# Kernel tuning notes

Hardware: AMD Instinct MI355X
Metric: run time of the kernel (lower is better)

Reference implementation:

```python
import jax, jax.numpy as jnp
import numpy as np
import math

B, C, H, W = 32, 3, 512, 512
K = 16
OUT_H, OUT_W = 512, 512

def _ctrl_pts(k):
    gs = int(math.sqrt(k))
    lin = jnp.linspace(-1.0, 1.0, gs)
    gy, gx = jnp.meshgrid(lin, lin, indexing='ij')
    return jnp.stack([gx, gy], axis=-1).reshape(-1, 2)

def setup_inputs() -> dict:
    key = jax.random.key(0)
    k1, k2, k3, k4 = jax.random.split(key, 4)
    x = jax.random.normal(k1, (B, C, H, W), jnp.float32)
    conv_w = jax.random.normal(k2, (8, C, 7, 7), jnp.float32) * 0.05
    conv_b = jax.random.normal(k3, (8,), jnp.float32) * 0.05
    fc_w = jax.random.normal(k4, (2 * K, 8), jnp.float32) * 0.01
    fc_b = jnp.asarray(_ctrl_pts(K).reshape(-1))  # module inits bias to ctrl grid
    return {"x": x, "conv_w": conv_w, "conv_b": conv_b, "fc_w": fc_w, "fc_b": fc_b}

def _U(sq):
    # U(r) = r^2 * log(r^2 + 1e-6), expressed with squared distance sq = r^2
    return sq * jnp.log(sq + 1e-6)

def _tps_grid(src, tgt, out_h, out_w):
    # src: [K,2] shared across batch (fixed ctrl grid), tgt: [B,K,2]
    Bb, Kk, _ = tgt.shape
    lin_y = jnp.linspace(-1.0, 1.0, out_h)
    lin_x = jnp.linspace(-1.0, 1.0, out_w)
    gy, gx = jnp.meshgrid(lin_y, lin_x, indexing='ij')
    grid = jnp.stack([gx, gy], axis=-1).reshape(-1, 2)  # [N,2]
    N = out_h * out_w
    # RBF kernel between output grid and source ctrl pts: [N,K]
    d2 = jnp.sum((grid[:, None, :] - src[None, :, :]) ** 2, axis=-1)
    U = _U(d2)
    # TPS system matrix L [K+3,K+3]; src is batch-shared so build it once
    src_d2 = jnp.sum((src[:, None, :] - src[None, :, :]) ** 2, axis=-1)
    P = jnp.concatenate([jnp.ones((Kk, 1)), src], axis=1)  # [K,3]
    L = jnp.zeros((Kk + 3, Kk + 3))
    L = L.at[:Kk, :Kk].set(_U(src_d2))
    L = L.at[:Kk, Kk:].set(P)
    L = L.at[Kk:, :Kk].set(P.T)
    Y = jnp.concatenate([tgt, jnp.zeros((Bb, 3, 2))], axis=1)  # [B,K+3,2]
    Wmat = jnp.linalg.solve(L[None], Y)  # [B,K+3,2]
    Pg = jnp.concatenate([jnp.ones((N, 1)), grid], axis=1)  # [N,3]
    mapped = (jnp.einsum('nk,bkc->bnc', U, Wmat[:, :Kk])
              + jnp.einsum('np,bpc->bnc', Pg, Wmat[:, Kk:]))
    return mapped.reshape(Bb, out_h, out_w, 2)

def _grid_sample(x, grid):
    # bilinear, zero padding, align_corners=False (torch defaults)
    Bb, Cc, Hh, Ww = x.shape
    ix = ((grid[..., 0] + 1.0) * Ww - 1.0) * 0.5
    iy = ((grid[..., 1] + 1.0) * Hh - 1.0) * 0.5
    x0 = jnp.floor(ix)
    y0 = jnp.floor(iy)
    wx1 = ix - x0
    wy1 = iy - y0
    x0i = x0.astype(jnp.int32)
    y0i = y0.astype(jnp.int32)

    def gather(img, yy, xx):
        valid = ((yy >= 0) & (yy < Hh) & (xx >= 0) & (xx < Ww)).astype(img.dtype)
        yc = jnp.clip(yy, 0, Hh - 1)
        xc = jnp.clip(xx, 0, Ww - 1)
        return img[:, yc, xc] * valid[None]

    def per(img, x0i, y0i, wx1, wy1):
        wx0 = 1.0 - wx1
        wy0 = 1.0 - wy1
        v00 = gather(img, y0i, x0i)
        v01 = gather(img, y0i, x0i + 1)
        v10 = gather(img, y0i + 1, x0i)
        v11 = gather(img, y0i + 1, x0i + 1)
        return (v00 * (wy0 * wx0)[None] + v01 * (wy0 * wx1)[None]
                + v10 * (wy1 * wx0)[None] + v11 * (wy1 * wx1)[None])

    return jax.vmap(per)(x, x0i, y0i, wx1, wy1)

def reference(x, conv_w, conv_b, fc_w, fc_b):
    # localization: conv7x7 -> relu -> global avg pool -> fc
    feat = jax.lax.conv_general_dilated(
        x, conv_w, window_strides=(1, 1), padding='VALID',
        dimension_numbers=('NCHW', 'OIHW', 'NCHW'))
    feat = jax.nn.relu(feat + conv_b[None, :, None, None])
    pooled = feat.mean(axis=(2, 3))  # [B,8] (AdaptiveAvgPool2d(1))
    pred = (pooled @ fc_w.T + fc_b).reshape(-1, K, 2)  # [B,K,2]
    src = _ctrl_pts(K)
    grid = _tps_grid(src, pred, OUT_H, OUT_W)  # [B,OUT_H,OUT_W,2]
    return _grid_sample(x, grid)
```

## Files before the change

kernel.cpp:

```cpp
#include <hip/hip_runtime.h>
#include <hip/hip_bf16.h>
#include <hip/hip_fp16.h>
#include <math.h>

#define BATCH 32
#define CH_IN 3
#define CH_OUT 8
#define IMG 512
#define KSZ 7
#define CONV_OUT 506
#define KPTS 16
#define TILES_PER_B 128

#define SROWS 23
#define PITCH_DW 76
#define SMEM_DW (CH_IN * SROWS * PITCH_DW)

#define BPB 8

typedef _Float16 half8_t __attribute__((ext_vector_type(8)));
typedef float f32x4_t __attribute__((ext_vector_type(4)));

__device__ __forceinline__ unsigned short f2h_bits(float f) {
    _Float16 h = (_Float16)f;
    unsigned short u;
    __builtin_memcpy(&u, &h, 2);
    return u;
}
__device__ __forceinline__ float h2f_bits(unsigned short u) {
    _Float16 h;
    __builtin_memcpy(&h, &u, 2);
    return (float)h;
}
__device__ __forceinline__ unsigned int pk2(float a, float b) {
    return (unsigned int)f2h_bits(a) | ((unsigned int)f2h_bits(b) << 16);
}

__global__ void wprep_kernel(const float* __restrict__ w, uint4* __restrict__ afrag) {
    int idx = blockIdx.x * 256 + threadIdx.x;
    if (idx >= 6 * 64) return;
    int s = idx >> 6, l = idx & 63;
    int m = l & 15;
    int dlt = m >> 3, o = m & 7;
    int oct = s * 4 + (l >> 4);
    int c = oct >> 3, ky = oct & 7;
    unsigned short h[8];
    #pragma unroll
    for (int j = 0; j < 8; ++j) {
        int kx = j - dlt;
        float v = 0.f;
        if (ky < KSZ && kx >= 0 && kx < KSZ)
            v = w[((o * CH_IN + c) * KSZ + ky) * KSZ + kx];
        h[j] = f2h_bits(v);
    }
    uint4 out;
    __builtin_memcpy(&out, h, 16);
    afrag[idx] = out;
}

template <bool FUSED>
__global__ __launch_bounds__(256)
void conv_pool_kernel(const float* __restrict__ x, unsigned short* __restrict__ xh,
                      const uint4* __restrict__ afrag, const float* __restrict__ conv_b,
                      float* __restrict__ partial) {
    __shared__ unsigned int smem[SMEM_DW];
    __shared__ float red[4][8];

    int blk = blockIdx.x;
    int b = blk >> 7;
    int stripe = (blk >> 2) & 31;
    int chunk = blk & 3;
    int ybase = stripe * 16;
    int x0 = chunk * 128;
    int tid = threadIdx.x;

    if (FUSED) {
        const float* xb = x + (size_t)b * CH_IN * IMG * IMG;
        unsigned short* xhb = xh + (size_t)b * CH_IN * IMG * IMG;
        for (int idx4 = tid; idx4 < SMEM_DW / 4; idx4 += 256) {
            int c = idx4 / (SROWS * 19);
            int rem = idx4 - c * (SROWS * 19);
            int r = rem / 19;
            int u4 = rem - r * 19;
            int grow = ybase + r;
            int gcol = x0 + (u4 << 3);
            uint4 v = make_uint4(0u, 0u, 0u, 0u);
            if (grow < IMG && gcol < IMG) {
                const float* rp = xb + ((size_t)c * IMG + grow) * IMG + gcol;
                float4 f0 = *(const float4*)rp;
                float4 f1 = *(const float4*)(rp + 4);
                v.x = pk2(f0.x, f0.y);
                v.y = pk2(f0.z, f0.w);
                v.z = pk2(f1.x, f1.y);
                v.w = pk2(f1.z, f1.w);
            }
            ((uint4*)smem)[idx4] = v;
            if (r < 16 && u4 < 16)
                *(uint4*)(xhb + ((size_t)c * IMG + grow) * IMG + gcol) = v;
        }
    } else {
        for (int idx = tid; idx < SMEM_DW; idx += 256) {
            int c = idx / (SROWS * PITCH_DW);
            int rem = idx - c * (SROWS * PITCH_DW);
            int r = rem / PITCH_DW;
            int u = rem - r * PITCH_DW;
            int grow = ybase + r, gcol = x0 + 2 * u;
            float f0 = 0.f, f1 = 0.f;
            if (grow < IMG) {
                const float* rp = x + (((size_t)b * CH_IN + c) * IMG + grow) * IMG;
                if (gcol < IMG) f0 = rp[gcol];
                if (gcol + 1 < IMG) f1 = rp[gcol + 1];
            }
            smem[idx] = pk2(f0, f1);
        }
    }
    __syncthreads();

    int l = tid & 63, w = tid >> 6;
    int n = l & 15, g = l >> 4;

    uint4 at[6];
    #pragma unroll
    for (int s = 0; s < 6; ++s) at[s] = afrag[s * 64 + l];

    int rowb[6];
    #pragma unroll
    for (int s = 0; s < 6; ++s) {
        int oct = s * 4 + g;
        int c = oct >> 3, ky = oct & 7;
        rowb[s] = (c * SROWS + n + ky) * (PITCH_DW * 4) + w * 64;
    }

    float bias_[4];
    {
        int ob = (g & 1) * 4;
        #pragma unroll
        for (int r2 = 0; r2 < 4; ++r2) bias_[r2] = conv_b[ob + r2];
    }
    bool rowok = (ybase + n) < CONV_OUT;
    int dlt = g >> 1;
    float sums[4] = {0.f, 0.f, 0.f, 0.f};
    const char* sb = (const char*)smem;

    #pragma unroll
    for (int u = 0; u < 4; ++u) {
        f32x4_t acc[4];
        #pragma unroll
        for (int d = 0; d < 4; ++d) acc[d] = (f32x4_t){0.f, 0.f, 0.f, 0.f};

        #pragma unroll
        for (int s = 0; s < 6; ++s) {
            uint4 lo = *(const uint4*)(sb + rowb[s] + (u << 4));
            uint4 hi = *(const uint4*)(sb + rowb[s] + (u << 4) + 16);
            unsigned int eu[8] = {lo.x, lo.y, lo.z, lo.w, hi.x, hi.y, hi.z, hi.w};
            half8_t a;
            __builtin_memcpy(&a, &at[s], 16);
            #pragma unroll
            for (int d = 0; d < 4; ++d) {
                uint4 bu = make_uint4(eu[d], eu[d + 1], eu[d + 2], eu[d + 3]);
                half8_t bf;
                __builtin_memcpy(&bf, &bu, 16);
                acc[d] = __builtin_amdgcn_mfma_f32_16x16x32_f16(a, bf, acc[d], 0, 0, 0);
            }
        }

        #pragma unroll
        for (int d = 0; d < 4; ++d) {
            int col = x0 + 32 * w + 8 * u + 2 * d + dlt;
            bool colok = col < CONV_OUT;
            #pragma unroll
            for (int r2 = 0; r2 < 4; ++r2) {
                float v = acc[d][r2] + bias_[r2];
                v = v > 0.f ? v : 0.f;
                sums[r2] += (rowok && colok) ? v : 0.f;
            }
        }
    }

    #pragma unroll
    for (int r2 = 0; r2 < 4; ++r2) {
        sums[r2] += __shfl_xor(sums[r2], 1, 64);
        sums[r2] += __shfl_xor(sums[r2], 2, 64);
        sums[r2] += __shfl_xor(sums[r2], 4, 64);
        sums[r2] += __shfl_xor(sums[r2], 8, 64);
        sums[r2] += __shfl_xor(sums[r2], 32, 64);
    }
    if (l == 0) {
        #pragma unroll
        for (int r2 = 0; r2 < 4; ++r2) red[w][r2] = sums[r2];
    }
    if (l == 16) {
        #pragma unroll
        for (int r2 = 0; r2 < 4; ++r2) red[w][4 + r2] = sums[r2];
    }
    __syncthreads();
    if (tid < CH_OUT) {
        float s = red[0][tid] + red[1][tid] + red[2][tid] + red[3][tid];
        partial[tid * (BATCH * TILES_PER_B) + b * TILES_PER_B + stripe * 4 + chunk] = s;
    }
}

__device__ __forceinline__ double ctrl_lin(int i) { return -1.0 + (2.0 / 3.0) * i; }

__global__ void solve_kernel(const float* __restrict__ partial,
                             const float* __restrict__ fc_w,
                             const float* __restrict__ fc_b,
                             float* __restrict__ Wf) {
    __shared__ double L[19][19];
    __shared__ double Ys[19][64];
    __shared__ double piv_fac[19];
    __shared__ int piv_idx;
    __shared__ float pooledS[BATCH][CH_OUT];

    int t = threadIdx.x;

    for (int p = t; p < BATCH * CH_OUT; p += 64) {
        int b = p >> 3, o = p & 7;
        const float4* pp = (const float4*)(partial + o * (BATCH * TILES_PER_B) + b * TILES_PER_B);
        double a0 = 0.0, a1 = 0.0, a2 = 0.0, a3 = 0.0;
        #pragma unroll
        for (int gq = 0; gq < TILES_PER_B / 4; ++gq) {
            float4 v = pp[gq];
            a0 += (double)v.x; a1 += (double)v.y;
            a2 += (double)v.z; a3 += (double)v.w;
        }
        pooledS[b][o] = (float)(((a0 + a1) + (a2 + a3)) / ((double)CONV_OUT * (double)CONV_OUT));
    }
    __syncthreads();

    {
        int b = t >> 1, c = t & 1;
        for (int k = 0; k < KPTS; ++k) {
            int j = k * 2 + c;
            double s = (double)fc_b[j];
            for (int o = 0; o < CH_OUT; ++o)
                s += (double)pooledS[b][o] * (double)fc_w[j * CH_OUT + o];
            Ys[k][t] = s;
        }
        for (int k = KPTS; k < 19; ++k) Ys[k][t] = 0.0;
    }

    for (int p = t; p < 19 * 19; p += 64) {
        int r = p / 19, cc = p % 19;
        double v;
        if (r < KPTS && cc < KPTS) {
            double dx = ctrl_lin(r & 3) - ctrl_lin(cc & 3);
            double dy = ctrl_lin(r >> 2) - ctrl_lin(cc >> 2);
            double d2 = dx * dx + dy * dy;
            v = d2 * log(d2 + 1e-6);
        } else if (r < KPTS) {
            v = (cc == KPTS) ? 1.0 : (cc == KPTS + 1 ? ctrl_lin(r & 3) : ctrl_lin(r >> 2));
        } else if (cc < KPTS) {
            v = (r == KPTS) ? 1.0 : (r == KPTS + 1 ? ctrl_lin(cc & 3) : ctrl_lin(cc >> 2));
        } else v = 0.0;
        L[r][cc] = v;
    }
    __syncthreads();

    for (int k = 0; k < 19; ++k) {
        if (t == 0) {
            int pi = k; double mx = fabs(L[k][k]);
            for (int i = k + 1; i < 19; ++i) {
                double a = fabs(L[i][k]);
                if (a > mx) { mx = a; pi = i; }
            }
            piv_idx = pi;
        }
        __syncthreads();
        int pi = piv_idx;
        if (pi != k) {
            if (t < 19) { double tmp = L[k][t]; L[k][t] = L[pi][t]; L[pi][t] = tmp; }
            { double tmp = Ys[k][t]; Ys[k][t] = Ys[pi][t]; Ys[pi][t] = tmp; }
        }
        __syncthreads();
        if (t > k && t < 19) piv_fac[t] = L[t][k] / L[k][k];
        __syncthreads();
        if (t > k && t < 19) {
            double lkj = L[k][t];
            for (int i = k + 1; i < 19; ++i) L[i][t] -= piv_fac[i] * lkj;
        }
        {
            double ykt = Ys[k][t];
            for (int i = k + 1; i < 19; ++i) Ys[i][t] -= piv_fac[i] * ykt;
        }
        __syncthreads();
    }

    for (int k = 18; k >= 0; --k) {
        double s = Ys[k][t];
        for (int j = k + 1; j < 19; ++j) s -= L[k][j] * Ys[j][t];
        Ys[k][t] = s / L[k][k];
    }

    {
        int b = t >> 1, c = t & 1;
        for (int k = 0; k < 19; ++k)
            Wf[(b * 19 + k) * 2 + c] = (float)Ys[k][t];
    }
}

template <bool H16>
__global__ __launch_bounds__(256)
void tps_sample_kernel(const float* __restrict__ x, const unsigned short* __restrict__ xh,
                       const float* __restrict__ Wf, float* __restrict__ out) {
    int blk = blockIdx.x;
    int bgrp = blk >> 10;
    int pix = ((blk & 1023) << 8) | threadIdx.x;
    int i = pix >> 9, j = pix & 511;

    float gx = -1.f + (2.f / 511.f) * (float)j;
    float gy = -1.f + (2.f / 511.f) * (float)i;

    float U[KPTS];
    #pragma unroll
    for (int k = 0; k < KPTS; ++k) {
        float sx = -1.f + (2.f / 3.f) * (float)(k & 3);
        float sy = -1.f + (2.f / 3.f) * (float)(k >> 2);
        float dx = gx - sx, dy = gy - sy;
        float d2 = dx * dx + dy * dy;
        U[k] = d2 * (0.69314718055994531f * __log2f(d2 + 1e-6f));
    }

    for (int b = bgrp * BPB; b < bgrp * BPB + BPB; ++b) {
        const float* Wb = Wf + b * 38;

        float mx = Wb[32] + gx * Wb[34] + gy * Wb[36];
        float my = Wb[33] + gx * Wb[35] + gy * Wb[37];
        #pragma unroll
        for (int k = 0; k < KPTS; ++k) {
            mx += U[k] * Wb[2 * k];
            my += U[k] * Wb[2 * k + 1];
        }

        float ix = (mx + 1.f) * 256.f - 0.5f;
        float iy = (my + 1.f) * 256.f - 0.5f;
        float x0f = floorf(ix), y0f = floorf(iy);
        int x0 = (int)x0f, y0 = (int)y0f;
        int x1 = x0 + 1, y1 = y0 + 1;
        float wx1 = ix - x0f, wy1 = iy - y0f;
        float wx0 = 1.f - wx1, wy0 = 1.f - wy1;

        bool vx0 = (x0 >= 0) & (x0 < IMG), vx1 = (x1 >= 0) & (x1 < IMG);
        bool vy0 = (y0 >= 0) & (y0 < IMG), vy1 = (y1 >= 0) & (y1 < IMG);
        int xc0 = min(max(x0, 0), IMG - 1), xc1 = min(max(x1, 0), IMG - 1);
        int yc0 = min(max(y0, 0), IMG - 1), yc1 = min(max(y1, 0), IMG - 1);

        float w00 = (vy0 && vx0) ? wy0 * wx0 : 0.f;
        float w01 = (vy0 && vx1) ? wy0 * wx1 : 0.f;
        float w10 = (vy1 && vx0) ? wy1 * wx0 : 0.f;
        float w11 = (vy1 && vx1) ? wy1 * wx1 : 0.f;

        int o00 = yc0 * IMG + xc0, o01 = yc0 * IMG + xc1;
        int o10 = yc1 * IMG + xc0, o11 = yc1 * IMG + xc1;

        #pragma unroll
        for (int c = 0; c < CH_IN; ++c) {
            float v;
            if (H16) {
                const unsigned short* xp = xh + ((size_t)b * CH_IN + c) * IMG * IMG;
                v = h2f_bits(xp[o00]) * w00 + h2f_bits(xp[o01]) * w01
                  + h2f_bits(xp[o10]) * w10 + h2f_bits(xp[o11]) * w11;
            } else {
                const float* xp = x + ((size_t)b * CH_IN + c) * IMG * IMG;
                v = xp[o00] * w00 + xp[o01] * w01 + xp[o10] * w10 + xp[o11] * w11;
            }
            out[(((size_t)b * CH_IN + c) << 18) + (i << 9) + j] = v;
        }
    }
}

extern "C" void kernel_launch(void* const* d_in, const int* in_sizes, int n_in,
                              void* d_out, int out_size, void* d_ws, size_t ws_size,
                              hipStream_t stream) {
    const float* x      = (const float*)d_in[0];
    const float* conv_w = (const float*)d_in[1];
    const float* conv_b = (const float*)d_in[2];
    const float* fc_w   = (const float*)d_in[3];
    const float* fc_b   = (const float*)d_in[4];
    float* out = (float*)d_out;

    char* ws = (char*)d_ws;
    uint4* afrag   = (uint4*)ws;
    float* partial = (float*)(ws + 8192);
    float* Wf      = (float*)(ws + 139264);
    unsigned short* xh = (unsigned short*)(ws + 147456);
    const size_t need = 147456 + (size_t)BATCH * CH_IN * IMG * IMG * 2;
    bool fused = ws_size >= need;

    wprep_kernel<<<dim3(2), dim3(256), 0, stream>>>(conv_w, afrag);
    if (fused) {
        conv_pool_kernel<true><<<dim3(BATCH * TILES_PER_B), dim3(256), 0, stream>>>(
            x, xh, afrag, conv_b, partial);
    } else {
        conv_pool_kernel<false><<<dim3(BATCH * TILES_PER_B), dim3(256), 0, stream>>>(
            x, xh, afrag, conv_b, partial);
    }
    solve_kernel<<<dim3(1), dim3(64), 0, stream>>>(partial, fc_w, fc_b, Wf);
    if (fused) {
        tps_sample_kernel<true><<<dim3(4 * 1024), dim3(256), 0, stream>>>(x, xh, Wf, out);
    } else {
        tps_sample_kernel<false><<<dim3(4 * 1024), dim3(256), 0, stream>>>(x, xh, Wf, out);
    }
}
```

Before: 145.5 us.

## Double-buffer conv input tiles across column chunks within one block per stripe

Each conv block now covers a whole 16-row stripe, walking its four 128-column chunks in turn instead of using one block per chunk. While the MFMA work runs on the current chunk, the next chunk's global loads go into registers and are written into a second shared-memory buffer. The aim is to hide global load latency behind compute and to cut launch and halo overhead, at the cost of four times fewer blocks, twice the LDS, and more registers for staging. The row pitch shrinks to 68 dwords and the partial-sum layout drops from 128 to 32 entries per batch.

```diff
diff --git a/kernel.cpp b/kernel.cpp
--- a/kernel.cpp
+++ b/kernel.cpp
@@ -10,11 +10,14 @@
 #define KSZ 7
 #define CONV_OUT 506
 #define KPTS 16
-#define TILES_PER_B 128
+#define STRIPES 32
 
 #define SROWS 23
-#define PITCH_DW 76
+#define PITCH_DW 68
+#define ROW_U4 17
 #define SMEM_DW (CH_IN * SROWS * PITCH_DW)
+#define NCHUNK (SMEM_DW / 4)
+#define NIT 5
 
 #define BPB 8
 
@@ -58,62 +61,73 @@
     afrag[idx] = out;
 }
 
+__device__ __forceinline__ void stage_load(const float* __restrict__ xb, int ybase,
+                                           int x0, int tid, float4* st) {
+    #pragma unroll
+    for (int it = 0; it < NIT; ++it) {
+        int idx4 = it * 256 + tid;
+        int i4 = idx4 < NCHUNK ? idx4 : 0;
+        int c = i4 / (SROWS * ROW_U4);
+        int rem = i4 - c * (SROWS * ROW_U4);
+        int r = rem / ROW_U4;
+        int u4 = rem - r * ROW_U4;
+        int grow = ybase + r;
+        int gcol = x0 + (u4 << 3);
+        int growc = grow < IMG ? grow : IMG - 1;
+        int gcolc = gcol < IMG ? gcol : IMG - 8;
+        const float* rp = xb + ((size_t)c * IMG + growc) * IMG + gcolc;
+        st[2 * it]     = *(const float4*)rp;
+        st[2 * it + 1] = *(const float4*)(rp + 4);
+    }
+}
+
 template <bool FUSED>
-__global__ __launch_bounds__(256)
+__device__ __forceinline__ void stage_write(const float4* st, unsigned int* __restrict__ dst,
+                                            unsigned short* __restrict__ xhb,
+                                            int ybase, int x0, int tid) {
+    #pragma unroll
+    for (int it = 0; it < NIT; ++it) {
+        int idx4 = it * 256 + tid;
+        bool ok = idx4 < NCHUNK;
+        int i4 = ok ? idx4 : 0;
+        int c = i4 / (SROWS * ROW_U4);
+        int rem = i4 - c * (SROWS * ROW_U4);
+        int r = rem / ROW_U4;
+        int u4 = rem - r * ROW_U4;
+        int grow = ybase + r;
+        int gcol = x0 + (u4 << 3);
+        bool inb = (grow < IMG) && (gcol < IMG);
+        float4 f0 = st[2 * it], f1 = st[2 * it + 1];
+        uint4 v;
+        v.x = inb ? pk2(f0.x, f0.y) : 0u;
+        v.y = inb ? pk2(f0.z, f0.w) : 0u;
+        v.z = inb ? pk2(f1.x, f1.y) : 0u;
+        v.w = inb ? pk2(f1.z, f1.w) : 0u;
+        if (ok) *(uint4*)(dst + i4 * 4) = v;
+        if (FUSED && ok && r < 16 && u4 < 16)
+            *(uint4*)(xhb + ((size_t)c * IMG + grow) * IMG + gcol) = v;
+    }
+}
+
+template <bool FUSED>
+__global__ __launch_bounds__(256, 4)
 void conv_pool_kernel(const float* __restrict__ x, unsigned short* __restrict__ xh,
                       const uint4* __restrict__ afrag, const float* __restrict__ conv_b,
                       float* __restrict__ partial) {
-    __shared__ unsigned int smem[SMEM_DW];
+    __shared__ unsigned int smem[2][SMEM_DW];
     __shared__ float red[4][8];
 
     int blk = blockIdx.x;
-    int b = blk >> 7;
-    int stripe = (blk >> 2) & 31;
-    int chunk = blk & 3;
+    int b = blk >> 5;
+    int stripe = blk & 31;
     int ybase = stripe * 16;
-    int x0 = chunk * 128;
     int tid = threadIdx.x;
-
-    if (FUSED) {
-        const float* xb = x + (size_t)b * CH_IN * IMG * IMG;
-        unsigned short* xhb = xh + (size_t)b * CH_IN * IMG * IMG;
-        for (int idx4 = tid; idx4 < SMEM_DW / 4; idx4 += 256) {
-            int c = idx4 / (SROWS * 19);
-            int rem = idx4 - c * (SROWS * 19);
-            int r = rem / 19;
-            int u4 = rem - r * 19;
-            int grow = ybase + r;
-            int gcol = x0 + (u4 << 3);
-            uint4 v = make_uint4(0u, 0u, 0u, 0u);
-            if (grow < IMG && gcol < IMG) {
-                const float* rp = xb + ((size_t)c * IMG + grow) * IMG + gcol;
-                float4 f0 = *(const float4*)rp;
-                float4 f1 = *(const float4*)(rp + 4);
-                v.x = pk2(f0.x, f0.y);
-                v.y = pk2(f0.z, f0.w);
-                v.z = pk2(f1.x, f1.y);
-                v.w = pk2(f1.z, f1.w);
-            }
-            ((uint4*)smem)[idx4] = v;
-            if (r < 16 && u4 < 16)
-                *(uint4*)(xhb + ((size_t)c * IMG + grow) * IMG + gcol) = v;
-        }
-    } else {
-        for (int idx = tid; idx < SMEM_DW; idx += 256) {
-            int c = idx / (SROWS * PITCH_DW);
-            int rem = idx - c * (SROWS * PITCH_DW);
-            int r = rem / PITCH_DW;
-            int u = rem - r * PITCH_DW;
-            int grow = ybase + r, gcol = x0 + 2 * u;
-            float f0 = 0.f, f1 = 0.f;
-            if (grow < IMG) {
-                const float* rp = x + (((size_t)b * CH_IN + c) * IMG + grow) * IMG;
-                if (gcol < IMG) f0 = rp[gcol];
-                if (gcol + 1 < IMG) f1 = rp[gcol + 1];
-            }
-            smem[idx] = pk2(f0, f1);
-        }
-    }
+    const float* xb = x + (size_t)b * CH_IN * IMG * IMG;
+    unsigned short* xhb = xh + (size_t)b * CH_IN * IMG * IMG;
+
+    float4 st[2 * NIT];
+    stage_load(xb, ybase, 0, tid, st);
+    stage_write<FUSED>(st, smem[0], xhb, ybase, 0, tid);
     __syncthreads();
 
     int l = tid & 63, w = tid >> 6;
@@ -140,40 +154,52 @@
     bool rowok = (ybase + n) < CONV_OUT;
     int dlt = g >> 1;
     float sums[4] = {0.f, 0.f, 0.f, 0.f};
-    const char* sb = (const char*)smem;
-
-    #pragma unroll
-    for (int u = 0; u < 4; ++u) {
-        f32x4_t acc[4];
-        #pragma unroll
-        for (int d = 0; d < 4; ++d) acc[d] = (f32x4_t){0.f, 0.f, 0.f, 0.f};
-
-        #pragma unroll
-        for (int s = 0; s < 6; ++s) {
-            uint4 lo = *(const uint4*)(sb + rowb[s] + (u << 4));
-            uint4 hi = *(const uint4*)(sb + rowb[s] + (u << 4) + 16);
-            unsigned int eu[8] = {lo.x, lo.y, lo.z, lo.w, hi.x, hi.y, hi.z, hi.w};
-            half8_t a;
-            __builtin_memcpy(&a, &at[s], 16);
+
+    int cur = 0;
+    #pragma unroll
+    for (int cc = 0; cc < 4; ++cc) {
+        if (cc < 3) stage_load(xb, ybase, (cc + 1) * 128, tid, st);
+
+        const char* sb = (const char*)smem[cur];
+        #pragma unroll
+        for (int u = 0; u < 4; ++u) {
+            f32x4_t acc[4];
+            #pragma unroll
+            for (int d = 0; d < 4; ++d) acc[d] = (f32x4_t){0.f, 0.f, 0.f, 0.f};
+
+            #pragma unroll
+            for (int s = 0; s < 6; ++s) {
+                uint4 lo = *(const uint4*)(sb + rowb[s] + (u << 4));
+                uint4 hi = *(const uint4*)(sb + rowb[s] + (u << 4) + 16);
+                unsigned int eu[8] = {lo.x, lo.y, lo.z, lo.w, hi.x, hi.y, hi.z, hi.w};
+                half8_t a;
+                __builtin_memcpy(&a, &at[s], 16);
+                #pragma unroll
+                for (int d = 0; d < 4; ++d) {
+                    uint4 bu = make_uint4(eu[d], eu[d + 1], eu[d + 2], eu[d + 3]);
+                    half8_t bf;
+                    __builtin_memcpy(&bf, &bu, 16);
+                    acc[d] = __builtin_amdgcn_mfma_f32_16x16x32_f16(a, bf, acc[d], 0, 0, 0);
+                }
+            }
+
             #pragma unroll
             for (int d = 0; d < 4; ++d) {
-                uint4 bu = make_uint4(eu[d], eu[d + 1], eu[d + 2], eu[d + 3]);
-                half8_t bf;
-                __builtin_memcpy(&bf, &bu, 16);
-                acc[d] = __builtin_amdgcn_mfma_f32_16x16x32_f16(a, bf, acc[d], 0, 0, 0);
+                int col = cc * 128 + 32 * w + 8 * u + 2 * d + dlt;
+                bool colok = col < CONV_OUT;
+                #pragma unroll
+                for (int r2 = 0; r2 < 4; ++r2) {
+                    float v = acc[d][r2] + bias_[r2];
+                    v = v > 0.f ? v : 0.f;
+                    sums[r2] += (rowok && colok) ? v : 0.f;
+                }
             }
         }
 
-        #pragma unroll
-        for (int d = 0; d < 4; ++d) {
-            int col = x0 + 32 * w + 8 * u + 2 * d + dlt;
-            bool colok = col < CONV_OUT;
-            #pragma unroll
-            for (int r2 = 0; r2 < 4; ++r2) {
-                float v = acc[d][r2] + bias_[r2];
-                v = v > 0.f ? v : 0.f;
-                sums[r2] += (rowok && colok) ? v : 0.f;
-            }
+        if (cc < 3) {
+            stage_write<FUSED>(st, smem[cur ^ 1], xhb, ybase, (cc + 1) * 128, tid);
+            __syncthreads();
+            cur ^= 1;
         }
     }
 
@@ -196,7 +222,7 @@
     __syncthreads();
     if (tid < CH_OUT) {
         float s = red[0][tid] + red[1][tid] + red[2][tid] + red[3][tid];
-        partial[tid * (BATCH * TILES_PER_B) + b * TILES_PER_B + stripe * 4 + chunk] = s;
+        partial[tid * (BATCH * STRIPES) + b * STRIPES + stripe] = s;
     }
 }
 
@@ -216,10 +242,10 @@
 
     for (int p = t; p < BATCH * CH_OUT; p += 64) {
         int b = p >> 3, o = p & 7;
-        const float4* pp = (const float4*)(partial + o * (BATCH * TILES_PER_B) + b * TILES_PER_B);
+        const float4* pp = (const float4*)(partial + o * (BATCH * STRIPES) + b * STRIPES);
         double a0 = 0.0, a1 = 0.0, a2 = 0.0, a3 = 0.0;
         #pragma unroll
-        for (int gq = 0; gq < TILES_PER_B / 4; ++gq) {
+        for (int gq = 0; gq < STRIPES / 4; ++gq) {
             float4 v = pp[gq];
             a0 += (double)v.x; a1 += (double)v.y;
             a2 += (double)v.z; a3 += (double)v.w;
@@ -389,10 +415,10 @@
 
     wprep_kernel<<<dim3(2), dim3(256), 0, stream>>>(conv_w, afrag);
     if (fused) {
-        conv_pool_kernel<true><<<dim3(BATCH * TILES_PER_B), dim3(256), 0, stream>>>(
+        conv_pool_kernel<true><<<dim3(BATCH * STRIPES), dim3(256), 0, stream>>>(
             x, xh, afrag, conv_b, partial);
     } else {
-        conv_pool_kernel<false><<<dim3(BATCH * TILES_PER_B), dim3(256), 0, stream>>>(
+        conv_pool_kernel<false><<<dim3(BATCH * STRIPES), dim3(256), 0, stream>>>(
             x, xh, afrag, conv_b, partial);
     }
     solve_kernel<<<dim3(1), dim3(64), 0, stream>>>(partial, fc_w, fc_b, Wf);
```

Result: slower. 210.3 us (+44.6%).
